# Kernel optimization log

Hardware: AMD Instinct MI355X
Metric: run time of the kernel (lower is better)

The kernel has to match this reference:

```python
import jax, jax.numpy as jnp
import numpy as np

S, X, G = 2048, 2048, 2
INPUT_SIZE = (3, 32, 32)
F = int(np.prod(INPUT_SIZE))


def setup_inputs() -> dict:
    key = jax.random.key(0)
    k1, k2, k3 = jax.random.split(key, 3)
    samples = jax.random.normal(k1, (S,) + INPUT_SIZE, dtype=jnp.float32)
    x = jax.random.normal(k2, (X,) + INPUT_SIZE, dtype=jnp.float32)
    # per-feature std per gradation, kept in [0.1, 1.0) like ranges_std scaling
    std = jax.random.uniform(k3, (G, F), dtype=jnp.float32, minval=0.1, maxval=1.0)
    return {"samples": samples, "x": x, "std": std}


def reference(samples, x, std):
    # samples: [S, C, H, W], x: [X, C, H, W], std: [G, F]
    G_, F_ = std.shape
    s = samples.reshape(samples.shape[0], F_)  # [S, F]
    xf = x.reshape(x.shape[0], F_)             # [X, F]
    w = 1.0 / (std * std)                       # [G, F] precision
    # per-gradation normalizer: -0.5*F*log(2pi) - sum_f log(std)
    const = -0.5 * F_ * jnp.log(2.0 * jnp.pi) - jnp.sum(jnp.log(std), axis=1)  # [G]
    # sum_f -0.5*((s-x)/std)^2 expanded: -0.5*(s^2 w - 2 s w x + x^2 w)
    A = jnp.einsum('sf,gf->gs', s * s, w)        # [G, S]
    C = jnp.einsum('xf,gf->gx', xf * xf, w)      # [G, X]
    B = jnp.einsum('sf,gf,xf->gsx', s, w, xf)    # [G, S, X] cross term
    logits = -0.5 * (A[:, :, None] - 2.0 * B + C[:, None, :]) + const[:, None, None]
    lp = jax.nn.logsumexp(logits, axis=2)        # over x (mixture components)
    lp = jax.nn.logsumexp(lp, axis=0)            # over gradations
    return lp - jnp.log(jnp.float32(x.shape[0] * G_))
```

## Files before the change

### kernel.cpp

```cpp
#include <hip/hip_runtime.h>
#include <math.h>
#include <stdint.h>

#define S_N 2048
#define X_N 2048
#define G_N 2
#define F_N 3072

#define TM 256
#define TN 128
#define BK 64
#define ITERS (F_N / BK)
#define NBUF 3

typedef __bf16 bf16;
typedef __bf16 bf16x4 __attribute__((ext_vector_type(4)));
typedef __bf16 bf16x8 __attribute__((ext_vector_type(8)));
typedef float f32x4 __attribute__((ext_vector_type(4)));
typedef int i32x4 __attribute__((ext_vector_type(4)));

__device__ __forceinline__ void gload_lds16(const bf16* g, void* l) {
  __builtin_amdgcn_global_load_lds(
      (const __attribute__((address_space(1))) void*)g,
      (__attribute__((address_space(3))) void*)l, 16, 0, 0);
}

__global__ __launch_bounds__(512) void k_prep(
    const float* __restrict__ samples, const float* __restrict__ xin,
    const float* __restrict__ stdv,
    bf16* __restrict__ U, bf16* __restrict__ V,
    float* __restrict__ A, float* __restrict__ C) {
  __shared__ float rlds[6432];
  int t = threadIdx.x;
  int bid = blockIdx.x;
  int lane = t & 63, wv = t >> 6;

  for (int i = t; i < 2 * F_N; i += 512) rlds[i] = 1.0f / stdv[i];

  float sl0 = 0.f, sl1 = 0.f;
  for (int i = t; i < F_N; i += 512) {
    sl0 += logf(stdv[i]);
    sl1 += logf(stdv[F_N + i]);
  }
  for (int o = 32; o; o >>= 1) { sl0 += __shfl_xor(sl0, o); sl1 += __shfl_xor(sl1, o); }
  if (lane == 0) { rlds[6400 + wv] = sl0; rlds[6408 + wv] = sl1; }
  __syncthreads();
  float t0 = 0.f, t1 = 0.f;
#pragma unroll
  for (int w2 = 0; w2 < 8; ++w2) { t0 += rlds[6400 + w2]; t1 += rlds[6408 + w2]; }
  const float KLOG = -0.5f * (float)F_N * 1.8378770664093453f;
  float c0 = KLOG - t0, c1 = KLOG - t1;

  int l32 = t & 31;
  int rr = bid * 16 + (t >> 5);
  bool isS = rr < S_N;
  int rx = isS ? rr : rr - S_N;
  const float* src = isS ? samples + (size_t)rx * F_N : xin + (size_t)rx * F_N;
  bf16* d0 = isS ? U + (size_t)rx * F_N : V + (size_t)rx * F_N;
  bf16* d1 = isS ? U + ((size_t)S_N + rx) * F_N : V + ((size_t)X_N + rx) * F_N;
  float a0 = 0.f, a1 = 0.f;
#pragma unroll 4
  for (int k = 0; k < 24; ++k) {
    int c4 = l32 + k * 32;
    float4 sv = ((const float4*)src)[c4];
    float4 q0 = ((const float4*)rlds)[c4];
    float4 q1 = ((const float4*)rlds)[768 + c4];
    bf16x4 b0, b1;
    b0[0] = (bf16)(sv.x * q0.x); b0[1] = (bf16)(sv.y * q0.y);
    b0[2] = (bf16)(sv.z * q0.z); b0[3] = (bf16)(sv.w * q0.w);
    b1[0] = (bf16)(sv.x * q1.x); b1[1] = (bf16)(sv.y * q1.y);
    b1[2] = (bf16)(sv.z * q1.z); b1[3] = (bf16)(sv.w * q1.w);
    float f0 = (float)b0[0], f1 = (float)b0[1], f2 = (float)b0[2], f3 = (float)b0[3];
    a0 += f0 * f0 + f1 * f1 + f2 * f2 + f3 * f3;
    float h0 = (float)b1[0], h1 = (float)b1[1], h2 = (float)b1[2], h3 = (float)b1[3];
    a1 += h0 * h0 + h1 * h1 + h2 * h2 + h3 * h3;
    ((bf16x4*)d0)[c4] = b0;
    ((bf16x4*)d1)[c4] = b1;
  }
  for (int o = 16; o; o >>= 1) { a0 += __shfl_xor(a0, o); a1 += __shfl_xor(a1, o); }
  if (l32 == 0) {
    if (isS) { A[rx] = a0 - 2.f * c0; A[S_N + rx] = a1 - 2.f * c1; }
    else     { C[rx] = a0;            C[X_N + rx] = a1; }
  }
}

__global__ __launch_bounds__(512, 2) void k_gemm(const bf16* __restrict__ U, const bf16* __restrict__ V,
                                                 const float* __restrict__ A, const float* __restrict__ C,
                                                 float* __restrict__ logits) {
  __shared__ i32x4 lds[NBUF * 2048 + NBUF * 1024];
  i32x4* ldsA = lds;
  i32x4* ldsB = lds + NBUF * 2048;

  int t = threadIdx.x;
  int g = blockIdx.z;
  int bm = blockIdx.y * TM;
  int bn = blockIdx.x * TN;

  const bf16* Ub = U + ((size_t)g * S_N + bm) * F_N;
  const bf16* Vb = V + ((size_t)g * X_N + bn) * F_N;

  int wave = t >> 6, lane = t & 63;
  int pos = wave >> 1;
  int kh = wave & 1;
  int wm = pos >> 1;
  int wn = pos & 1;
  int r = lane & 15, q = lane >> 4;
  int fr = (r >> 1) & 7;
  int ck = (kh * 4 + q) ^ fr;
  int abase = (wm * 128 + r) * 8;
  int bbase = (wn * 64 + r) * 8;

  int row0 = t >> 3;
  int gcc = (t & 7) ^ ((t >> 4) & 7);
  const bf16* gA[4];
  const bf16* gB[2];
#pragma unroll
  for (int j = 0; j < 4; ++j) gA[j] = Ub + (size_t)(row0 + j * 64) * F_N + gcc * 8;
#pragma unroll
  for (int j = 0; j < 2; ++j) gB[j] = Vb + (size_t)(row0 + j * 64) * F_N + gcc * 8;

  f32x4 acc[8][4] = {};
  bf16x8 af[8], bfr[4];

#pragma unroll
  for (int j = 0; j < 4; ++j) gload_lds16(gA[j], &ldsA[0 * 2048 + t + j * 512]);
#pragma unroll
  for (int j = 0; j < 2; ++j) gload_lds16(gB[j], &ldsB[0 * 1024 + t + j * 512]);
#pragma unroll
  for (int j = 0; j < 4; ++j) gload_lds16(gA[j] + BK, &ldsA[1 * 2048 + t + j * 512]);
#pragma unroll
  for (int j = 0; j < 2; ++j) gload_lds16(gB[j] + BK, &ldsB[1 * 1024 + t + j * 512]);
  asm volatile("s_waitcnt vmcnt(6)" ::: "memory");
  __builtin_amdgcn_s_barrier();
  __builtin_amdgcn_sched_barrier(0);
#pragma unroll
  for (int ni = 0; ni < 4; ++ni)
    bfr[ni] = __builtin_bit_cast(bf16x8, ldsB[bbase + ni * 128 + ck]);
#pragma unroll
  for (int mi = 0; mi < 8; ++mi)
    af[mi] = __builtin_bit_cast(bf16x8, ldsA[abase + mi * 128 + ck]);

  int cur = 0;
  for (int it = 0; it < ITERS; ++it) {
    int k2 = it + 2;
    int pk = (k2 < ITERS ? k2 : 0) * BK;
    int stg = (cur >= 1) ? cur - 1 : 2;
    int nxt = (cur == 2) ? 0 : cur + 1;
    const i32x4* LAn = ldsA + nxt * 2048;
    const i32x4* LBn = ldsB + nxt * 1024;

    gload_lds16(gA[0] + pk, &ldsA[stg * 2048 + t]);
    gload_lds16(gA[1] + pk, &ldsA[stg * 2048 + t + 512]);
    gload_lds16(gA[2] + pk, &ldsA[stg * 2048 + t + 1024]);
    gload_lds16(gA[3] + pk, &ldsA[stg * 2048 + t + 1536]);
    gload_lds16(gB[0] + pk, &ldsB[stg * 1024 + t]);
    gload_lds16(gB[1] + pk, &ldsB[stg * 1024 + t + 512]);

    __builtin_amdgcn_s_setprio(1);
#pragma unroll
    for (int ni = 0; ni < 4; ++ni)
#pragma unroll
      for (int mi = 0; mi < 8; ++mi)
        acc[mi][ni] = __builtin_amdgcn_mfma_f32_16x16x32_bf16(af[mi], bfr[ni], acc[mi][ni], 0, 0, 0);
    __builtin_amdgcn_s_setprio(0);

    asm volatile("s_waitcnt vmcnt(6)" ::: "memory");
    __builtin_amdgcn_s_barrier();
    __builtin_amdgcn_sched_barrier(0);
#pragma unroll
    for (int ni = 0; ni < 4; ++ni)
      bfr[ni] = __builtin_bit_cast(bf16x8, LBn[bbase + ni * 128 + ck]);
#pragma unroll
    for (int mi = 0; mi < 8; ++mi)
      af[mi] = __builtin_bit_cast(bf16x8, LAn[abase + mi * 128 + ck]);

    cur = nxt;
  }

  asm volatile("s_waitcnt vmcnt(0) lgkmcnt(0)" ::: "memory");
  __builtin_amdgcn_s_barrier();

  f32x4* scr = (f32x4*)lds;
  {
    f32x4* mw = scr + wave * 1024;
    if (kh == 0) {
#pragma unroll
      for (int mi = 0; mi < 8; ++mi)
#pragma unroll
        for (int nl = 0; nl < 2; ++nl)
          mw[(mi * 2 + nl) * 64 + lane] = acc[mi][2 + nl];
    } else {
#pragma unroll
      for (int mi = 0; mi < 8; ++mi)
#pragma unroll
        for (int nl = 0; nl < 2; ++nl)
          mw[(mi * 2 + nl) * 64 + lane] = acc[mi][nl];
    }
  }
  __syncthreads();
  {
    const f32x4* pw = scr + (wave ^ 1) * 1024;
    if (kh == 0) {
#pragma unroll
      for (int mi = 0; mi < 8; ++mi)
#pragma unroll
        for (int nl = 0; nl < 2; ++nl)
          acc[mi][nl] += pw[(mi * 2 + nl) * 64 + lane];
    } else {
#pragma unroll
      for (int mi = 0; mi < 8; ++mi)
#pragma unroll
        for (int nl = 0; nl < 2; ++nl)
          acc[mi][2 + nl] += pw[(mi * 2 + nl) * 64 + lane];
    }
  }

  const float* Ap = A + (size_t)g * S_N + bm + wm * 128;
  const float* Cp = C + (size_t)g * X_N + bn + wn * 64 + kh * 32;
  float cv[2];
  cv[0] = Cp[r]; cv[1] = Cp[16 + r];
#pragma unroll
  for (int mi = 0; mi < 8; ++mi) {
#pragma unroll
    for (int i = 0; i < 4; ++i) {
      int rowl = mi * 16 + q * 4 + i;
      float av = Ap[rowl];
      float* orow = logits + ((size_t)g * S_N + bm + wm * 128 + rowl) * X_N + bn + wn * 64 + kh * 32;
      if (kh == 0) {
        orow[r]      = acc[mi][0][i] - 0.5f * (av + cv[0]);
        orow[16 + r] = acc[mi][1][i] - 0.5f * (av + cv[1]);
      } else {
        orow[r]      = acc[mi][2][i] - 0.5f * (av + cv[0]);
        orow[16 + r] = acc[mi][3][i] - 0.5f * (av + cv[1]);
      }
    }
  }
}

__global__ void k_lse(const float* __restrict__ logits, float* __restrict__ out) {
  int s = blockIdx.x, t = threadIdx.x;
  const float4* p0 = (const float4*)(logits + (size_t)s * X_N);
  const float4* p1 = (const float4*)(logits + ((size_t)S_N + s) * X_N);
  float4 v[4];
  v[0] = p0[t]; v[1] = p0[t + 256];
  v[2] = p1[t]; v[3] = p1[t + 256];

  float m = v[0].x;
#pragma unroll
  for (int j = 0; j < 4; ++j) {
    m = fmaxf(m, v[j].x); m = fmaxf(m, v[j].y);
    m = fmaxf(m, v[j].z); m = fmaxf(m, v[j].w);
  }
  for (int o = 32; o; o >>= 1) m = fmaxf(m, __shfl_xor(m, o));
  __shared__ float redm[4];
  __shared__ float reds[4];
  int w = t >> 6, l = t & 63;
  if (l == 0) redm[w] = m;
  __syncthreads();
  m = fmaxf(fmaxf(redm[0], redm[1]), fmaxf(redm[2], redm[3]));

  float sum = 0.f;
#pragma unroll
  for (int j = 0; j < 4; ++j) {
    sum += expf(v[j].x - m) + expf(v[j].y - m) + expf(v[j].z - m) + expf(v[j].w - m);
  }
  for (int o = 32; o; o >>= 1) sum += __shfl_xor(sum, o);
  if (l == 0) reds[w] = sum;
  __syncthreads();
  if (t == 0) {
    float tot = reds[0] + reds[1] + reds[2] + reds[3];
    out[s] = m + logf(tot) - 8.317766166719343f;
  }
}

extern "C" void kernel_launch(void* const* d_in, const int* in_sizes, int n_in,
                              void* d_out, int out_size, void* d_ws, size_t ws_size,
                              hipStream_t stream) {
  const float* samples = (const float*)d_in[0];
  const float* xin     = (const float*)d_in[1];
  const float* stdv    = (const float*)d_in[2];
  float* out = (float*)d_out;

  char* ws = (char*)d_ws;
  size_t off = 0;
  bf16* U = (bf16*)(ws + off);        off += (size_t)G_N * S_N * F_N * 2;
  bf16* V = (bf16*)(ws + off);        off += (size_t)G_N * X_N * F_N * 2;
  float* logits = (float*)(ws + off); off += (size_t)G_N * S_N * X_N * 4;
  float* A = (float*)(ws + off);      off += (size_t)G_N * S_N * 4;
  float* C = (float*)(ws + off);      off += (size_t)G_N * X_N * 4;

  k_prep<<<dim3(256), dim3(512), 0, stream>>>(samples, xin, stdv, U, V, A, C);
  k_gemm<<<dim3(X_N / TN, S_N / TM, G_N), dim3(512), 0, stream>>>(U, V, A, C, logits);
  k_lse<<<dim3(S_N), dim3(256), 0, stream>>>(logits, out);
}
```

Before: 158.6 us.

## Fuse prep, GEMM and logsumexp into one persistent kernel with grid barriers

Merges the three launches into a single 256-block kernel that separates the prep, GEMM and logsumexp phases with atomic-counter grid barriers. A memset resets the counters before each launch. The goal is to remove the inter-kernel launch gaps and tail drains. It relies on all 256 blocks being co-resident, which should hold with 2 blocks per CU on 256 CUs but risks deadlock otherwise. The spin barriers and the extra memset add their own overhead.

```diff
diff --git a/kernel.cpp b/kernel.cpp
--- a/kernel.cpp
+++ b/kernel.cpp
@@ -25,251 +25,253 @@
       (__attribute__((address_space(3))) void*)l, 16, 0, 0);
 }
 
-__global__ __launch_bounds__(512) void k_prep(
+__device__ __forceinline__ void gridbar(unsigned int* cnt) {
+  __syncthreads();
+  if (threadIdx.x == 0) {
+    __threadfence();
+    __hip_atomic_fetch_add(cnt, 1u, __ATOMIC_ACQ_REL, __HIP_MEMORY_SCOPE_AGENT);
+    while (__hip_atomic_load(cnt, __ATOMIC_ACQUIRE, __HIP_MEMORY_SCOPE_AGENT) < 256u) {
+      __builtin_amdgcn_s_sleep(8);
+    }
+  }
+  __syncthreads();
+}
+
+__global__ __launch_bounds__(512, 2) void k_mega(
     const float* __restrict__ samples, const float* __restrict__ xin,
     const float* __restrict__ stdv,
     bf16* __restrict__ U, bf16* __restrict__ V,
-    float* __restrict__ A, float* __restrict__ C) {
-  __shared__ float rlds[6432];
+    float* __restrict__ A, float* __restrict__ C,
+    float* __restrict__ logits, float* __restrict__ out,
+    unsigned int* __restrict__ sync) {
+  __shared__ i32x4 lds[NBUF * 2048 + NBUF * 1024];
   int t = threadIdx.x;
   int bid = blockIdx.x;
-  int lane = t & 63, wv = t >> 6;
-
-  for (int i = t; i < 2 * F_N; i += 512) rlds[i] = 1.0f / stdv[i];
-
-  float sl0 = 0.f, sl1 = 0.f;
-  for (int i = t; i < F_N; i += 512) {
-    sl0 += logf(stdv[i]);
-    sl1 += logf(stdv[F_N + i]);
-  }
-  for (int o = 32; o; o >>= 1) { sl0 += __shfl_xor(sl0, o); sl1 += __shfl_xor(sl1, o); }
-  if (lane == 0) { rlds[6400 + wv] = sl0; rlds[6408 + wv] = sl1; }
-  __syncthreads();
-  float t0 = 0.f, t1 = 0.f;
-#pragma unroll
-  for (int w2 = 0; w2 < 8; ++w2) { t0 += rlds[6400 + w2]; t1 += rlds[6408 + w2]; }
-  const float KLOG = -0.5f * (float)F_N * 1.8378770664093453f;
-  float c0 = KLOG - t0, c1 = KLOG - t1;
-
-  int l32 = t & 31;
-  int rr = bid * 16 + (t >> 5);
-  bool isS = rr < S_N;
-  int rx = isS ? rr : rr - S_N;
-  const float* src = isS ? samples + (size_t)rx * F_N : xin + (size_t)rx * F_N;
-  bf16* d0 = isS ? U + (size_t)rx * F_N : V + (size_t)rx * F_N;
-  bf16* d1 = isS ? U + ((size_t)S_N + rx) * F_N : V + ((size_t)X_N + rx) * F_N;
-  float a0 = 0.f, a1 = 0.f;
+
+  {
+    float* rlds = (float*)lds;
+    int lane = t & 63, wv = t >> 6;
+    for (int i = t; i < 2 * F_N; i += 512) rlds[i] = 1.0f / stdv[i];
+
+    float sl0 = 0.f, sl1 = 0.f;
+    for (int i = t; i < F_N; i += 512) {
+      sl0 += logf(stdv[i]);
+      sl1 += logf(stdv[F_N + i]);
+    }
+    for (int o = 32; o; o >>= 1) { sl0 += __shfl_xor(sl0, o); sl1 += __shfl_xor(sl1, o); }
+    if (lane == 0) { rlds[6400 + wv] = sl0; rlds[6408 + wv] = sl1; }
+    __syncthreads();
+    float t0 = 0.f, t1 = 0.f;
+#pragma unroll
+    for (int w2 = 0; w2 < 8; ++w2) { t0 += rlds[6400 + w2]; t1 += rlds[6408 + w2]; }
+    const float KLOG = -0.5f * (float)F_N * 1.8378770664093453f;
+    float c0 = KLOG - t0, c1 = KLOG - t1;
+
+    int l32 = t & 31;
+    int rr = bid * 16 + (t >> 5);
+    bool isS = rr < S_N;
+    int rx = isS ? rr : rr - S_N;
+    const float* src = isS ? samples + (size_t)rx * F_N : xin + (size_t)rx * F_N;
+    bf16* d0 = isS ? U + (size_t)rx * F_N : V + (size_t)rx * F_N;
+    bf16* d1 = isS ? U + ((size_t)S_N + rx) * F_N : V + ((size_t)X_N + rx) * F_N;
+    float a0 = 0.f, a1 = 0.f;
 #pragma unroll 4
-  for (int k = 0; k < 24; ++k) {
-    int c4 = l32 + k * 32;
-    float4 sv = ((const float4*)src)[c4];
-    float4 q0 = ((const float4*)rlds)[c4];
-    float4 q1 = ((const float4*)rlds)[768 + c4];
-    bf16x4 b0, b1;
-    b0[0] = (bf16)(sv.x * q0.x); b0[1] = (bf16)(sv.y * q0.y);
-    b0[2] = (bf16)(sv.z * q0.z); b0[3] = (bf16)(sv.w * q0.w);
-    b1[0] = (bf16)(sv.x * q1.x); b1[1] = (bf16)(sv.y * q1.y);
-    b1[2] = (bf16)(sv.z * q1.z); b1[3] = (bf16)(sv.w * q1.w);
-    float f0 = (float)b0[0], f1 = (float)b0[1], f2 = (float)b0[2], f3 = (float)b0[3];
-    a0 += f0 * f0 + f1 * f1 + f2 * f2 + f3 * f3;
-    float h0 = (float)b1[0], h1 = (float)b1[1], h2 = (float)b1[2], h3 = (float)b1[3];
-    a1 += h0 * h0 + h1 * h1 + h2 * h2 + h3 * h3;
-    ((bf16x4*)d0)[c4] = b0;
-    ((bf16x4*)d1)[c4] = b1;
-  }
-  for (int o = 16; o; o >>= 1) { a0 += __shfl_xor(a0, o); a1 += __shfl_xor(a1, o); }
-  if (l32 == 0) {
-    if (isS) { A[rx] = a0 - 2.f * c0; A[S_N + rx] = a1 - 2.f * c1; }
-    else     { C[rx] = a0;            C[X_N + rx] = a1; }
-  }
-}
-
-__global__ __launch_bounds__(512, 2) void k_gemm(const bf16* __restrict__ U, const bf16* __restrict__ V,
-                                                 const float* __restrict__ A, const float* __restrict__ C,
-                                                 float* __restrict__ logits) {
-  __shared__ i32x4 lds[NBUF * 2048 + NBUF * 1024];
-  i32x4* ldsA = lds;
-  i32x4* ldsB = lds + NBUF * 2048;
-
-  int t = threadIdx.x;
-  int g = blockIdx.z;
-  int bm = blockIdx.y * TM;
-  int bn = blockIdx.x * TN;
-
-  const bf16* Ub = U + ((size_t)g * S_N + bm) * F_N;
-  const bf16* Vb = V + ((size_t)g * X_N + bn) * F_N;
-
-  int wave = t >> 6, lane = t & 63;
-  int pos = wave >> 1;
-  int kh = wave & 1;
-  int wm = pos >> 1;
-  int wn = pos & 1;
-  int r = lane & 15, q = lane >> 4;
-  int fr = (r >> 1) & 7;
-  int ck = (kh * 4 + q) ^ fr;
-  int abase = (wm * 128 + r) * 8;
-  int bbase = (wn * 64 + r) * 8;
-
-  int row0 = t >> 3;
-  int gcc = (t & 7) ^ ((t >> 4) & 7);
-  const bf16* gA[4];
-  const bf16* gB[2];
-#pragma unroll
-  for (int j = 0; j < 4; ++j) gA[j] = Ub + (size_t)(row0 + j * 64) * F_N + gcc * 8;
-#pragma unroll
-  for (int j = 0; j < 2; ++j) gB[j] = Vb + (size_t)(row0 + j * 64) * F_N + gcc * 8;
-
-  f32x4 acc[8][4] = {};
-  bf16x8 af[8], bfr[4];
-
-#pragma unroll
-  for (int j = 0; j < 4; ++j) gload_lds16(gA[j], &ldsA[0 * 2048 + t + j * 512]);
-#pragma unroll
-  for (int j = 0; j < 2; ++j) gload_lds16(gB[j], &ldsB[0 * 1024 + t + j * 512]);
-#pragma unroll
-  for (int j = 0; j < 4; ++j) gload_lds16(gA[j] + BK, &ldsA[1 * 2048 + t + j * 512]);
-#pragma unroll
-  for (int j = 0; j < 2; ++j) gload_lds16(gB[j] + BK, &ldsB[1 * 1024 + t + j * 512]);
-  asm volatile("s_waitcnt vmcnt(6)" ::: "memory");
-  __builtin_amdgcn_s_barrier();
-  __builtin_amdgcn_sched_barrier(0);
-#pragma unroll
-  for (int ni = 0; ni < 4; ++ni)
-    bfr[ni] = __builtin_bit_cast(bf16x8, ldsB[bbase + ni * 128 + ck]);
-#pragma unroll
-  for (int mi = 0; mi < 8; ++mi)
-    af[mi] = __builtin_bit_cast(bf16x8, ldsA[abase + mi * 128 + ck]);
-
-  int cur = 0;
-  for (int it = 0; it < ITERS; ++it) {
-    int k2 = it + 2;
-    int pk = (k2 < ITERS ? k2 : 0) * BK;
-    int stg = (cur >= 1) ? cur - 1 : 2;
-    int nxt = (cur == 2) ? 0 : cur + 1;
-    const i32x4* LAn = ldsA + nxt * 2048;
-    const i32x4* LBn = ldsB + nxt * 1024;
-
-    gload_lds16(gA[0] + pk, &ldsA[stg * 2048 + t]);
-    gload_lds16(gA[1] + pk, &ldsA[stg * 2048 + t + 512]);
-    gload_lds16(gA[2] + pk, &ldsA[stg * 2048 + t + 1024]);
-    gload_lds16(gA[3] + pk, &ldsA[stg * 2048 + t + 1536]);
-    gload_lds16(gB[0] + pk, &ldsB[stg * 1024 + t]);
-    gload_lds16(gB[1] + pk, &ldsB[stg * 1024 + t + 512]);
-
-    __builtin_amdgcn_s_setprio(1);
-#pragma unroll
-    for (int ni = 0; ni < 4; ++ni)
-#pragma unroll
-      for (int mi = 0; mi < 8; ++mi)
-        acc[mi][ni] = __builtin_amdgcn_mfma_f32_16x16x32_bf16(af[mi], bfr[ni], acc[mi][ni], 0, 0, 0);
-    __builtin_amdgcn_s_setprio(0);
-
+    for (int k = 0; k < 24; ++k) {
+      int c4 = l32 + k * 32;
+      float4 sv = ((const float4*)src)[c4];
+      float4 q0 = ((const float4*)rlds)[c4];
+      float4 q1 = ((const float4*)rlds)[768 + c4];
+      bf16x4 b0, b1;
+      b0[0] = (bf16)(sv.x * q0.x); b0[1] = (bf16)(sv.y * q0.y);
+      b0[2] = (bf16)(sv.z * q0.z); b0[3] = (bf16)(sv.w * q0.w);
+      b1[0] = (bf16)(sv.x * q1.x); b1[1] = (bf16)(sv.y * q1.y);
+      b1[2] = (bf16)(sv.z * q1.z); b1[3] = (bf16)(sv.w * q1.w);
+      float f0 = (float)b0[0], f1 = (float)b0[1], f2 = (float)b0[2], f3 = (float)b0[3];
+      a0 += f0 * f0 + f1 * f1 + f2 * f2 + f3 * f3;
+      float h0 = (float)b1[0], h1 = (float)b1[1], h2 = (float)b1[2], h3 = (float)b1[3];
+      a1 += h0 * h0 + h1 * h1 + h2 * h2 + h3 * h3;
+      ((bf16x4*)d0)[c4] = b0;
+      ((bf16x4*)d1)[c4] = b1;
+    }
+    for (int o = 16; o; o >>= 1) { a0 += __shfl_xor(a0, o); a1 += __shfl_xor(a1, o); }
+    if (l32 == 0) {
+      if (isS) { A[rx] = a0 - 2.f * c0; A[S_N + rx] = a1 - 2.f * c1; }
+      else     { C[rx] = a0;            C[X_N + rx] = a1; }
+    }
+  }
+  gridbar(sync + 0);
+
+  {
+    i32x4* ldsA = lds;
+    i32x4* ldsB = lds + NBUF * 2048;
+
+    int bx = bid & 15, by = (bid >> 4) & 7, g = bid >> 7;
+    int bm = by * TM, bn = bx * TN;
+
+    const bf16* Ub = U + ((size_t)g * S_N + bm) * F_N;
+    const bf16* Vb = V + ((size_t)g * X_N + bn) * F_N;
+
+    int wave = t >> 6, lane = t & 63;
+    int pos = wave >> 1;
+    int kh = wave & 1;
+    int wm = pos >> 1;
+    int wn = pos & 1;
+    int r = lane & 15, q = lane >> 4;
+    int fr = (r >> 1) & 7;
+    int ck = (kh * 4 + q) ^ fr;
+    int abase = (wm * 128 + r) * 8;
+    int bbase = (wn * 64 + r) * 8;
+
+    int row0 = t >> 3;
+    int gcc = (t & 7) ^ ((t >> 4) & 7);
+    const bf16* gA[4];
+    const bf16* gB[2];
+#pragma unroll
+    for (int j = 0; j < 4; ++j) gA[j] = Ub + (size_t)(row0 + j * 64) * F_N + gcc * 8;
+#pragma unroll
+    for (int j = 0; j < 2; ++j) gB[j] = Vb + (size_t)(row0 + j * 64) * F_N + gcc * 8;
+
+    f32x4 acc[8][4] = {};
+    bf16x8 af[8], bfr[4];
+
+#pragma unroll
+    for (int j = 0; j < 4; ++j) gload_lds16(gA[j], &ldsA[0 * 2048 + t + j * 512]);
+#pragma unroll
+    for (int j = 0; j < 2; ++j) gload_lds16(gB[j], &ldsB[0 * 1024 + t + j * 512]);
+#pragma unroll
+    for (int j = 0; j < 4; ++j) gload_lds16(gA[j] + BK, &ldsA[1 * 2048 + t + j * 512]);
+#pragma unroll
+    for (int j = 0; j < 2; ++j) gload_lds16(gB[j] + BK, &ldsB[1 * 1024 + t + j * 512]);
     asm volatile("s_waitcnt vmcnt(6)" ::: "memory");
     __builtin_amdgcn_s_barrier();
     __builtin_amdgcn_sched_barrier(0);
 #pragma unroll
     for (int ni = 0; ni < 4; ++ni)
-      bfr[ni] = __builtin_bit_cast(bf16x8, LBn[bbase + ni * 128 + ck]);
+      bfr[ni] = __builtin_bit_cast(bf16x8, ldsB[bbase + ni * 128 + ck]);
 #pragma unroll
     for (int mi = 0; mi < 8; ++mi)
-      af[mi] = __builtin_bit_cast(bf16x8, LAn[abase + mi * 128 + ck]);
-
-    cur = nxt;
-  }
-
-  asm volatile("s_waitcnt vmcnt(0) lgkmcnt(0)" ::: "memory");
-  __builtin_amdgcn_s_barrier();
-
-  f32x4* scr = (f32x4*)lds;
+      af[mi] = __builtin_bit_cast(bf16x8, ldsA[abase + mi * 128 + ck]);
+
+    int cur = 0;
+    for (int it = 0; it < ITERS; ++it) {
+      int k2 = it + 2;
+      int pk = (k2 < ITERS ? k2 : 0) * BK;
+      int stg = (cur >= 1) ? cur - 1 : 2;
+      int nxt = (cur == 2) ? 0 : cur + 1;
+      const i32x4* LAn = ldsA + nxt * 2048;
+      const i32x4* LBn = ldsB + nxt * 1024;
+
+      gload_lds16(gA[0] + pk, &ldsA[stg * 2048 + t]);
+      gload_lds16(gA[1] + pk, &ldsA[stg * 2048 + t + 512]);
+      gload_lds16(gA[2] + pk, &ldsA[stg * 2048 + t + 1024]);
+      gload_lds16(gA[3] + pk, &ldsA[stg * 2048 + t + 1536]);
+      gload_lds16(gB[0] + pk, &ldsB[stg * 1024 + t]);
+      gload_lds16(gB[1] + pk, &ldsB[stg * 1024 + t + 512]);
+
+      __builtin_amdgcn_s_setprio(1);
+#pragma unroll
+      for (int ni = 0; ni < 4; ++ni)
+#pragma unroll
+        for (int mi = 0; mi < 8; ++mi)
+          acc[mi][ni] = __builtin_amdgcn_mfma_f32_16x16x32_bf16(af[mi], bfr[ni], acc[mi][ni], 0, 0, 0);
+      __builtin_amdgcn_s_setprio(0);
+
+      asm volatile("s_waitcnt vmcnt(6)" ::: "memory");
+      __builtin_amdgcn_s_barrier();
+      __builtin_amdgcn_sched_barrier(0);
+#pragma unroll
+      for (int ni = 0; ni < 4; ++ni)
+        bfr[ni] = __builtin_bit_cast(bf16x8, LBn[bbase + ni * 128 + ck]);
+#pragma unroll
+      for (int mi = 0; mi < 8; ++mi)
+        af[mi] = __builtin_bit_cast(bf16x8, LAn[abase + mi * 128 + ck]);
+
+      cur = nxt;
+    }
+
+    asm volatile("s_waitcnt vmcnt(0) lgkmcnt(0)" ::: "memory");
+    __builtin_amdgcn_s_barrier();
+
+    f32x4* scr = (f32x4*)lds;
+    {
+      f32x4* mw = scr + wave * 1024;
+      if (kh == 0) {
+#pragma unroll
+        for (int mi = 0; mi < 8; ++mi)
+#pragma unroll
+          for (int nl = 0; nl < 2; ++nl)
+            mw[(mi * 2 + nl) * 64 + lane] = acc[mi][2 + nl];
+      } else {
+#pragma unroll
+        for (int mi = 0; mi < 8; ++mi)
+#pragma unroll
+          for (int nl = 0; nl < 2; ++nl)
+            mw[(mi * 2 + nl) * 64 + lane] = acc[mi][nl];
+      }
+    }
+    __syncthreads();
+    {
+      const f32x4* pw = scr + (wave ^ 1) * 1024;
+      if (kh == 0) {
+#pragma unroll
+        for (int mi = 0; mi < 8; ++mi)
+#pragma unroll
+          for (int nl = 0; nl < 2; ++nl)
+            acc[mi][nl] += pw[(mi * 2 + nl) * 64 + lane];
+      } else {
+#pragma unroll
+        for (int mi = 0; mi < 8; ++mi)
+#pragma unroll
+          for (int nl = 0; nl < 2; ++nl)
+            acc[mi][2 + nl] += pw[(mi * 2 + nl) * 64 + lane];
+      }
+    }
+
+    const float* Ap = A + (size_t)g * S_N + bm + wm * 128;
+    const float* Cp = C + (size_t)g * X_N + bn + wn * 64 + kh * 32;
+    float cv[2];
+    cv[0] = Cp[r]; cv[1] = Cp[16 + r];
+#pragma unroll
+    for (int mi = 0; mi < 8; ++mi) {
+#pragma unroll
+      for (int i = 0; i < 4; ++i) {
+        int rowl = mi * 16 + q * 4 + i;
+        float av = Ap[rowl];
+        float* orow = logits + ((size_t)g * S_N + bm + wm * 128 + rowl) * X_N + bn + wn * 64 + kh * 32;
+        if (kh == 0) {
+          orow[r]      = acc[mi][0][i] - 0.5f * (av + cv[0]);
+          orow[16 + r] = acc[mi][1][i] - 0.5f * (av + cv[1]);
+        } else {
+          orow[r]      = acc[mi][2][i] - 0.5f * (av + cv[0]);
+          orow[16 + r] = acc[mi][3][i] - 0.5f * (av + cv[1]);
+        }
+      }
+    }
+  }
+  gridbar(sync + 1);
+
   {
-    f32x4* mw = scr + wave * 1024;
-    if (kh == 0) {
-#pragma unroll
-      for (int mi = 0; mi < 8; ++mi)
-#pragma unroll
-        for (int nl = 0; nl < 2; ++nl)
-          mw[(mi * 2 + nl) * 64 + lane] = acc[mi][2 + nl];
-    } else {
-#pragma unroll
-      for (int mi = 0; mi < 8; ++mi)
-#pragma unroll
-        for (int nl = 0; nl < 2; ++nl)
-          mw[(mi * 2 + nl) * 64 + lane] = acc[mi][nl];
-    }
-  }
-  __syncthreads();
-  {
-    const f32x4* pw = scr + (wave ^ 1) * 1024;
-    if (kh == 0) {
-#pragma unroll
-      for (int mi = 0; mi < 8; ++mi)
-#pragma unroll
-        for (int nl = 0; nl < 2; ++nl)
-          acc[mi][nl] += pw[(mi * 2 + nl) * 64 + lane];
-    } else {
-#pragma unroll
-      for (int mi = 0; mi < 8; ++mi)
-#pragma unroll
-        for (int nl = 0; nl < 2; ++nl)
-          acc[mi][2 + nl] += pw[(mi * 2 + nl) * 64 + lane];
-    }
-  }
-
-  const float* Ap = A + (size_t)g * S_N + bm + wm * 128;
-  const float* Cp = C + (size_t)g * X_N + bn + wn * 64 + kh * 32;
-  float cv[2];
-  cv[0] = Cp[r]; cv[1] = Cp[16 + r];
-#pragma unroll
-  for (int mi = 0; mi < 8; ++mi) {
-#pragma unroll
-    for (int i = 0; i < 4; ++i) {
-      int rowl = mi * 16 + q * 4 + i;
-      float av = Ap[rowl];
-      float* orow = logits + ((size_t)g * S_N + bm + wm * 128 + rowl) * X_N + bn + wn * 64 + kh * 32;
-      if (kh == 0) {
-        orow[r]      = acc[mi][0][i] - 0.5f * (av + cv[0]);
-        orow[16 + r] = acc[mi][1][i] - 0.5f * (av + cv[1]);
-      } else {
-        orow[r]      = acc[mi][2][i] - 0.5f * (av + cv[0]);
-        orow[16 + r] = acc[mi][3][i] - 0.5f * (av + cv[1]);
-      }
-    }
-  }
-}
-
-__global__ void k_lse(const float* __restrict__ logits, float* __restrict__ out) {
-  int s = blockIdx.x, t = threadIdx.x;
-  const float4* p0 = (const float4*)(logits + (size_t)s * X_N);
-  const float4* p1 = (const float4*)(logits + ((size_t)S_N + s) * X_N);
-  float4 v[4];
-  v[0] = p0[t]; v[1] = p0[t + 256];
-  v[2] = p1[t]; v[3] = p1[t + 256];
-
-  float m = v[0].x;
-#pragma unroll
-  for (int j = 0; j < 4; ++j) {
-    m = fmaxf(m, v[j].x); m = fmaxf(m, v[j].y);
-    m = fmaxf(m, v[j].z); m = fmaxf(m, v[j].w);
-  }
-  for (int o = 32; o; o >>= 1) m = fmaxf(m, __shfl_xor(m, o));
-  __shared__ float redm[4];
-  __shared__ float reds[4];
-  int w = t >> 6, l = t & 63;
-  if (l == 0) redm[w] = m;
-  __syncthreads();
-  m = fmaxf(fmaxf(redm[0], redm[1]), fmaxf(redm[2], redm[3]));
-
-  float sum = 0.f;
-#pragma unroll
-  for (int j = 0; j < 4; ++j) {
-    sum += expf(v[j].x - m) + expf(v[j].y - m) + expf(v[j].z - m) + expf(v[j].w - m);
-  }
-  for (int o = 32; o; o >>= 1) sum += __shfl_xor(sum, o);
-  if (l == 0) reds[w] = sum;
-  __syncthreads();
-  if (t == 0) {
-    float tot = reds[0] + reds[1] + reds[2] + reds[3];
-    out[s] = m + logf(tot) - 8.317766166719343f;
+    int wv = t >> 6, l = t & 63;
+    int s = bid * 8 + wv;
+    const float4* p0 = (const float4*)(logits + (size_t)s * X_N);
+    const float4* p1 = (const float4*)(logits + ((size_t)S_N + s) * X_N);
+    float4 v[16];
+#pragma unroll
+    for (int k = 0; k < 8; ++k) { v[k] = p0[l + k * 64]; v[8 + k] = p1[l + k * 64]; }
+    float m = v[0].x;
+#pragma unroll
+    for (int k = 0; k < 16; ++k) {
+      m = fmaxf(m, v[k].x); m = fmaxf(m, v[k].y);
+      m = fmaxf(m, v[k].z); m = fmaxf(m, v[k].w);
+    }
+    for (int o = 32; o; o >>= 1) m = fmaxf(m, __shfl_xor(m, o));
+    float sum = 0.f;
+#pragma unroll
+    for (int k = 0; k < 16; ++k) {
+      sum += expf(v[k].x - m) + expf(v[k].y - m) + expf(v[k].z - m) + expf(v[k].w - m);
+    }
+    for (int o = 32; o; o >>= 1) sum += __shfl_xor(sum, o);
+    if (l == 0) out[s] = m + logf(sum) - 8.317766166719343f;
   }
 }
 
@@ -288,8 +290,9 @@
   float* logits = (float*)(ws + off); off += (size_t)G_N * S_N * X_N * 4;
   float* A = (float*)(ws + off);      off += (size_t)G_N * S_N * 4;
   float* C = (float*)(ws + off);      off += (size_t)G_N * X_N * 4;
-
-  k_prep<<<dim3(256), dim3(512), 0, stream>>>(samples, xin, stdv, U, V, A, C);
-  k_gemm<<<dim3(X_N / TN, S_N / TM, G_N), dim3(512), 0, stream>>>(U, V, A, C, logits);
-  k_lse<<<dim3(S_N), dim3(256), 0, stream>>>(logits, out);
-}
+  unsigned int* sync = (unsigned int*)(ws + off); off += 256;
+
+  hipMemsetAsync(sync, 0, 8, stream);
+  k_mega<<<dim3(256), dim3(512), 0, stream>>>(samples, xin, stdv, U, V, A, C,
+                                              logits, out, sync);
+}
```

Result: slower. 242.8 us (+53.1%).
